# Kernel optimization log

Hardware: AMD Instinct MI355X
Metric: run time of the kernel (lower is better)

Reference implementation:

```python
import jax, jax.numpy as jnp
import numpy as np


def sign_ste(x):
    # forward-only module: plain sign (STE only matters for backward)
    return jnp.sign(x)


def fake_quant8(w):
    # per-tensor abs-max int8 fake quantization (scale is a buffer, not differentiated)
    scale = jax.lax.stop_gradient(jnp.max(jnp.abs(w)) / 127.0 + 1e-8)
    q = jnp.clip(jnp.round(w / scale), -128.0, 127.0)
    return q * scale


def conv2d(x, w):
    # VALID 3x3 conv, NCHW / OIHW, no bias
    return jax.lax.conv_general_dilated(
        x, w, window_strides=(1, 1), padding='VALID',
        dimension_numbers=('NCHW', 'OIHW', 'NCHW'))


def avg_pool2(x):
    # AvgPool2d(kernel=2, stride=2); spatial dims are even (22 -> 11)
    B, C, H, W = x.shape
    return x.reshape(B, C, H // 2, 2, W // 2, 2).mean(axis=(3, 5))


def setup_inputs() -> dict:
    key = jax.random.key(0)
    k = jax.random.split(key, 6)
    B = 8192
    x = jax.random.normal(k[0], (B, 1, 28, 28), dtype=jnp.float32)
    w1 = jax.random.normal(k[1], (16, 1, 3, 3), dtype=jnp.float32) * 0.1
    w2 = jax.random.normal(k[2], (16, 16, 3, 3), dtype=jnp.float32) * 0.1
    w3 = jax.random.normal(k[3], (32, 16, 3, 3), dtype=jnp.float32) * 0.1
    w_fc = jax.random.normal(k[4], (10, 32 * 11 * 11), dtype=jnp.float32) * 0.02
    b_fc = jax.random.normal(k[5], (10,), dtype=jnp.float32) * 0.02
    return {'x': x, 'w1': w1, 'w2': w2, 'w3': w3, 'w_fc': w_fc, 'b_fc': b_fc}


def reference(x, w1, w2, w3, w_fc, b_fc):
    h = fake_quant8(conv2d(x, w1))          # [B,16,26,26] int8 fake-quant
    h = sign_ste(h)                          # binarized activations
    h = sign_ste(conv2d(h, sign_ste(w2)))    # [B,16,24,24] binarized conv
    h = sign_ste(conv2d(h, sign_ste(w3)))    # [B,32,22,22] binarized conv
    h = avg_pool2(h)                         # [B,32,11,11]
    h = h.reshape(h.shape[0], -1)            # [B,3872]
    return h @ sign_ste(w_fc).T + b_fc       # [B,10]
```

## Files before the change

kernel.cpp:

```cpp
#include <hip/hip_runtime.h>
#include <stdint.h>


typedef int int4v __attribute__((ext_vector_type(4)));
typedef float f2 __attribute__((ext_vector_type(2)));

__device__ __forceinline__ int4v mfma_i8(int4v a, int4v b, int4v c) {
  return __builtin_amdgcn_mfma_i32_16x16x64_i8(a, b, c, 0, 0, 0);
}

__device__ __forceinline__ int dot4(int a, int b, int c) {
#if __has_builtin(__builtin_amdgcn_sdot4)
  return __builtin_amdgcn_sdot4(a, b, c, false);
#else
  int r = c;
  r += (int)(int8_t)(a)       * (int)(int8_t)(b);
  r += (int)(int8_t)(a >> 8)  * (int)(int8_t)(b >> 8);
  r += (int)(int8_t)(a >> 16) * (int)(int8_t)(b >> 16);
  r += (int)(int8_t)(a >> 24) * (int)(int8_t)(b >> 24);
  return r;
#endif
}

__device__ __forceinline__ int pack4(int r0, int r1, int r2, int r3) {
  const int t0 = __builtin_amdgcn_perm(r1, r0, 0x00000400);
  const int t1 = __builtin_amdgcn_perm(r3, r2, 0x00000400);
  return __builtin_amdgcn_perm(t1, t0, 0x05040100);
}

__device__ __forceinline__ int cl02(int v) {
  v = (v > 0) ? v : 0;
  v = (v < 2) ? v : 2;
  return v;
}

__device__ __forceinline__ int sgn_pack_byte(float v) {
  return (v > 0.f) - (v < 0.f);
}

__global__ __launch_bounds__(256) void k_prep_max(
    const float* __restrict__ x, const float* __restrict__ w1,
    const float* __restrict__ w2, const float* __restrict__ w3,
    const float* __restrict__ wfc, const float* __restrict__ bfc,
    int* __restrict__ ws, int B, int NMAX) {
  __shared__ __align__(16) float xs[1568];
  __shared__ __align__(8) float w1t[144];
  __shared__ float wred[4];
  __shared__ int part[4];

  const int tid = threadIdx.x;
  if ((int)blockIdx.x < NMAX) {
    const int img0 = blockIdx.x * 2;
    const bool has1 = (img0 + 1) < B;
    {
      const float4* x4a = (const float4*)(x + (size_t)img0 * 784);
      const float4* x4b = (const float4*)(x + (size_t)(img0 + (int)has1) * 784);
      for (int u = tid; u < 392; u += 256) {
        const int im = (u >= 196), i = im ? u - 196 : u;
        const float4 v = im ? x4b[i] : x4a[i];
        *(float4*)&xs[im * 784 + i * 4] = v;
      }
    }
    if (tid < 144) w1t[(tid % 9) * 16 + tid / 9] = w1[tid];
    __syncthreads();
    const f2* w1t2 = (const f2*)w1t;
    const float* xs0 = xs;
    const float* xs1 = xs + 784;
    float m = 0.f;
    for (int px = tid; px < 676; px += 256) {
      const int oy = px / 26, ox = px - oy * 26;
      float xw0[9], xw1[9];
#pragma unroll
      for (int r = 0; r < 3; ++r)
#pragma unroll
        for (int cc = 0; cc < 3; ++cc) {
          const int ix = (oy + r) * 28 + ox + cc;
          xw0[r * 3 + cc] = xs0[ix];
          xw1[r * 3 + cc] = xs1[ix];
        }
#pragma unroll
      for (int cw = 0; cw < 8; ++cw) {
        f2 h0 = {0.f, 0.f}, h1 = {0.f, 0.f};
#pragma unroll
        for (int i = 0; i < 9; ++i) {
          const f2 w = w1t2[i * 8 + cw];
          const f2 s0 = {xw0[i], xw0[i]};
          const f2 s1 = {xw1[i], xw1[i]};
          h0 += w * s0;
          h1 += w * s1;
        }
        m = fmaxf(m, fmaxf(fmaxf(fabsf(h0.x), fabsf(h0.y)),
                           fmaxf(fabsf(h1.x), fabsf(h1.y))));
      }
    }
#pragma unroll
    for (int off = 32; off; off >>= 1) m = fmaxf(m, __shfl_down(m, off, 64));
    if ((tid & 63) == 0) wred[tid >> 6] = m;
    __syncthreads();
    if (tid == 0) {
      const float mm = fmaxf(fmaxf(wred[0], wred[1]), fmaxf(wred[2], wred[3]));
      atomicMax(ws + ((int)blockIdx.x & 31), (int)__float_as_uint(mm));
    }
    return;
  }

  const int pb = blockIdx.x - NMAX;
  if (pb < 10) {
    const int j = pb;
    int s = 0;
    for (int i = tid; i < 3872; i += 256) {
      const float v = wfc[j * 3872 + i];
      s += (v > 0.f) - (v < 0.f);
    }
#pragma unroll
    for (int off = 32; off; off >>= 1) s += __shfl_down(s, off, 64);
    if ((tid & 63) == 0) part[tid >> 6] = s;
    __syncthreads();
    if (tid == 0) {
      const int rs = part[0] + part[1] + part[2] + part[3];
      ((float*)ws)[64 + j] = bfc[j] - (float)rs;
    }
    if (pb == 1 && tid < 16) {
      int s2 = 0;
      for (int i = 0; i < 144; ++i) s2 += sgn_pack_byte(w2[tid * 144 + i]);
      ws[80 + tid] = s2;
    }
    if (pb == 2 && tid < 32) {
      int s3 = 0;
      for (int i = 0; i < 144; ++i) s3 += sgn_pack_byte(w3[tid * 144 + i]);
      ws[96 + tid] = s3;
    }
    return;
  }
  int* dst = ws + 128;
  const int widx = (pb - 10) * 256 + tid;
  if (widx < 576) {
    const int oc = widx / 36, r = widx % 36, wp = r >> 2, icg = r & 3;
    unsigned wrd = 0;
#pragma unroll
    for (int b = 0; b < 4; ++b) {
      const float v = w2[(oc * 16 + icg * 4 + b) * 9 + wp];
      wrd |= ((unsigned)(uint8_t)(int8_t)sgn_pack_byte(v)) << (8 * b);
    }
    dst[widx] = (int)wrd;
  } else if (widx < 1728) {
    const int t = widx - 576;
    const int oc = t / 36, r = t % 36, wp = r >> 2, icg = r & 3;
    unsigned wrd = 0;
#pragma unroll
    for (int b = 0; b < 4; ++b) {
      const float v = w3[(oc * 16 + icg * 4 + b) * 9 + wp];
      wrd |= ((unsigned)(uint8_t)(int8_t)sgn_pack_byte(v)) << (8 * b);
    }
    dst[widx] = (int)wrd;
  } else if (widx < 11408) {
    const int t = widx - 1728;
    const int j = t / 968, r = t % 968, pos = r >> 3, cg = r & 7;
    unsigned wrd = 0;
#pragma unroll
    for (int b = 0; b < 4; ++b) {
      const float v = wfc[j * 3872 + (cg * 4 + b) * 121 + pos];
      wrd |= ((unsigned)(uint8_t)(int8_t)sgn_pack_byte(v)) << (8 * b);
    }
    dst[widx] = (int)wrd;
  }
}

__global__ __launch_bounds__(256) void k_forward(
    const float* __restrict__ x, const float* __restrict__ w1,
    const int* __restrict__ wsd,
    float* __restrict__ out, int B) {
  __shared__ __align__(16) char smem[40144];
  constexpr int RIMG = 20032;
  int* out_acc = (int*)(smem + 40064);

  const int* wpack = wsd + 128;
  const int* sw = wsd + 1856;
  const float* badj = (const float*)(wsd + 64);

  const int tid = threadIdx.x;
  const int img0 = blockIdx.x * 2;
  const bool has1 = (img0 + 1) < B;

  {
    const float4* x4a = (const float4*)(x + (size_t)img0 * 784);
    const float4* x4b = (const float4*)(x + (size_t)(img0 + (int)has1) * 784);
    for (int u = tid; u < 392; u += 256) {
      const int img = (u >= 196), i = img ? u - 196 : u;
      const float4 v = img ? x4b[i] : x4a[i];
      *(float4*)(smem + img * RIMG + 10816 + i * 16) = v;
    }
  }
  if (tid < 144) *(float*)(smem + 13952 + ((tid % 9) * 16 + tid / 9) * 4) = w1[tid];
  if (tid < 20) out_acc[tid] = 0;
  __syncthreads();

  float mraw = __uint_as_float((unsigned)wsd[0]);
#pragma unroll
  for (int k = 1; k < 32; ++k) mraw = fmaxf(mraw, __uint_as_float((unsigned)wsd[k]));
  const float scale = mraw / 127.0f + 1e-8f;
  const float thr = 0.5f * scale;
  const f2* w1t2 = (const f2*)(smem + 13952);
  const float* xs0 = (const float*)(smem + 10816);
  const float* xs1 = (const float*)(smem + RIMG + 10816);
  for (int px = tid; px < 676; px += 256) {
    const int oy = px / 26, ox = px - oy * 26;
    float xw0[9], xw1[9];
#pragma unroll
    for (int r = 0; r < 3; ++r)
#pragma unroll
      for (int cc = 0; cc < 3; ++cc) {
        const int ix = (oy + r) * 28 + ox + cc;
        xw0[r * 3 + cc] = xs0[ix];
        xw1[r * 3 + cc] = xs1[ix];
      }
    unsigned wq0[4] = {0u, 0u, 0u, 0u}, wq1[4] = {0u, 0u, 0u, 0u};
#pragma unroll
    for (int cw = 0; cw < 8; ++cw) {
      f2 h0 = {0.f, 0.f}, h1 = {0.f, 0.f};
#pragma unroll
      for (int i = 0; i < 9; ++i) {
        const f2 w = w1t2[i * 8 + cw];
        const f2 s0 = {xw0[i], xw0[i]};
        const f2 s1 = {xw1[i], xw1[i]};
        h0 += w * s0;
        h1 += w * s1;
      }
      wq0[cw >> 1] |= ((unsigned)((h0.x >= -thr) + (h0.x > thr))) << (8 * ((2 * cw) & 3));
      wq0[cw >> 1] |= ((unsigned)((h0.y >= -thr) + (h0.y > thr))) << (8 * ((2 * cw + 1) & 3));
      wq1[cw >> 1] |= ((unsigned)((h1.x >= -thr) + (h1.x > thr))) << (8 * ((2 * cw) & 3));
      wq1[cw >> 1] |= ((unsigned)((h1.y >= -thr) + (h1.y > thr))) << (8 * ((2 * cw + 1) & 3));
    }
    *(int4*)(smem + px * 16) =
        make_int4((int)wq0[0], (int)wq0[1], (int)wq0[2], (int)wq0[3]);
    *(int4*)(smem + RIMG + px * 16) =
        make_int4((int)wq1[0], (int)wq1[1], (int)wq1[2], (int)wq1[3]);
  }
  __syncthreads();

  const int lane = tid & 63, wv = tid >> 6;
  const int col = lane & 15, quad = lane >> 4;
  int dAct2[3], dAct3[3];
#pragma unroll
  for (int t = 0; t < 3; ++t) {
    const int wp = t * 4 + quad;
    dAct2[t] = ((wp / 3) * 26 + wp % 3) * 16;
    dAct3[t] = ((wp / 3) * 24 + wp % 3) * 16;
  }
  const bool kq0 = (quad == 0);

  {
    const int* wb = wpack + col * 36;
    int4v WA[3];
    WA[0] = *(const int4v*)(wb + quad * 4);
    WA[1] = *(const int4v*)(wb + 16 + quad * 4);
    WA[2] = kq0 ? *(const int4v*)(wb + 32) : (int4v){0, 0, 0, 0};
    const int4v acc0 = (int4v){1, 1, 1, 1} - *(const int4v*)(wsd + 80 + quad * 4);
#pragma unroll
    for (int img = 0; img < 2; ++img) {
      const int8_t* a1b = (const int8_t*)(smem + img * RIMG);
      int p0 = wv * 16 + col;
      int oy = p0 / 24, ox = p0 - oy * 24;
      const int8_t* abase = a1b + (oy * 26 + ox) * 16;
      int* h2p = (int*)(smem + img * RIMG + 10816 + p0 * 16 + quad * 4);
      for (int it = 0; it < 9; ++it) {
        int4v acc = acc0;
        acc = mfma_i8(WA[0], *(const int4v*)(abase + dAct2[0]), acc);
        acc = mfma_i8(WA[1], *(const int4v*)(abase + dAct2[1]), acc);
        acc = mfma_i8(WA[2], *(const int4v*)(abase + dAct2[2]), acc);
        *h2p = pack4(cl02(acc[0]), cl02(acc[1]), cl02(acc[2]), cl02(acc[3]));
        h2p += 256;
        abase += 1088;
        ox += 16;
        if (ox >= 24) { ox -= 24; abase += 32; }
      }
    }
  }
  __syncthreads();

  {
    int4v WA[2][3];
    int4v ac0[2];
#pragma unroll
    for (int ot = 0; ot < 2; ++ot) {
      const int* wb = wpack + 576 + (ot * 16 + col) * 36;
      WA[ot][0] = *(const int4v*)(wb + quad * 4);
      WA[ot][1] = *(const int4v*)(wb + 16 + quad * 4);
      WA[ot][2] = kq0 ? *(const int4v*)(wb + 32) : (int4v){0, 0, 0, 0};
      ac0[ot] = (int4v){1, 1, 1, 1} - *(const int4v*)(wsd + 96 + ot * 16 + quad * 4);
    }
    const int sub = col & 3;
    const int sy = sub >> 1, sx = sub & 1;
    const int cell0 = wv * 4 + (col >> 2);
    const int cy0 = cell0 / 11, cx0 = cell0 - cy0 * 11;
    const int aoff0 = ((cy0 * 2 + sy) * 24 + cx0 * 2 + sx) * 16;
    const int pb0 = cell0 * 8 + quad;
    const int aoffcap = ((20 + sy) * 24 + 20 + sx) * 16;
    const int pbcap = 120 * 8 + quad;
    const bool wlane = (sub == 0);
#pragma unroll
    for (int img = 0; img < 2; ++img) {
      const int8_t* h2b = (const int8_t*)(smem + img * RIMG + 10816);
      int* p4 = (int*)(smem + img * RIMG);
      int aoff = aoff0, pb = pb0, cx = cx0;
      for (int pt = wv; pt < 31; pt += 4) {
        const int8_t* abase = h2b + ((aoff < aoffcap) ? aoff : aoffcap);
        const int pbu = (pb < pbcap) ? pb : pbcap;
        const int4v B0 = *(const int4v*)(abase + dAct3[0]);
        const int4v B1 = *(const int4v*)(abase + dAct3[1]);
        const int4v B2 = *(const int4v*)(abase + dAct3[2]);
#pragma unroll
        for (int ot = 0; ot < 2; ++ot) {
          int4v acc = ac0[ot];
          acc = mfma_i8(WA[ot][0], B0, acc);
          acc = mfma_i8(WA[ot][1], B1, acc);
          acc = mfma_i8(WA[ot][2], B2, acc);
          int s = pack4(cl02(acc[0]), cl02(acc[1]), cl02(acc[2]), cl02(acc[3]));
          s += __builtin_amdgcn_update_dpp(0, s, 0xB1, 0xF, 0xF, false);
          s += __builtin_amdgcn_update_dpp(0, s, 0x4E, 0xF, 0xF, false);
          if (wlane) p4[pbu + ot * 4] = s;
        }
        aoff += 928;
        pb += 128;
        cx += 5;
        if (cx >= 11) { cx -= 11; aoff += 416; }
      }
    }
  }
  __syncthreads();

  for (int u = tid; u < 500; u += 256) {
    const int img = u / 250, r = u - img * 250;
    const int j = r / 25, k = r - j * 25;
    const int4* p44 = (const int4*)(smem + img * RIMG);
    int acc = 0;
    for (int pos = k; pos < 121; pos += 25) {
      const int4 pa = p44[pos * 2];
      const int4 pb = p44[pos * 2 + 1];
      const int* swr = sw + j * 968 + pos * 8;
      const int4 wa = *(const int4*)(swr);
      const int4 wbv = *(const int4*)(swr + 4);
      acc = dot4(pa.x, wa.x, acc);
      acc = dot4(pa.y, wa.y, acc);
      acc = dot4(pa.z, wa.z, acc);
      acc = dot4(pa.w, wa.w, acc);
      acc = dot4(pb.x, wbv.x, acc);
      acc = dot4(pb.y, wbv.y, acc);
      acc = dot4(pb.z, wbv.z, acc);
      acc = dot4(pb.w, wbv.w, acc);
    }
    atomicAdd(&out_acc[img * 10 + j], acc);
  }
  __syncthreads();
  if (tid < 20) {
    const int img = tid / 10, j = tid - img * 10;
    if (img == 0 || has1)
      out[(size_t)(img0 + img) * 10 + j] = 0.25f * (float)out_acc[tid] + badj[j];
  }
}

extern "C" void kernel_launch(void* const* d_in, const int* in_sizes, int n_in,
                              void* d_out, int out_size, void* d_ws, size_t ws_size,
                              hipStream_t stream) {
  const float* x   = (const float*)d_in[0];
  const float* w1  = (const float*)d_in[1];
  const float* w2  = (const float*)d_in[2];
  const float* w3  = (const float*)d_in[3];
  const float* wfc = (const float*)d_in[4];
  const float* bfc = (const float*)d_in[5];
  float* out = (float*)d_out;
  int* wsd = (int*)d_ws;
  const int B = in_sizes[0] / 784;
  const int NMAX = (B + 1) / 2;

  hipLaunchKernelGGL(k_prep_max, dim3(NMAX + 56), dim3(256), 0, stream,
                     x, w1, w2, w3, wfc, bfc, wsd, B, NMAX);
  hipLaunchKernelGGL(k_forward, dim3((B + 1) / 2), dim3(256), 0, stream, x, w1,
                     (const int*)wsd, out, B);
}
```

Measured before the change: 202.9 us.

## Process one image per block with halved LDS and padded conv2 output layout

Each block now processes one image instead of two, which halves shared memory (about 20KB) and doubles the grid so more blocks can be resident per CU. The conv1 loop is reordered to hold weights for one channel pair in registers across three pixel passes. The conv2 output row stride is padded from 24 to 25 positions, likely to reduce LDS bank conflicts in the conv3 reads. In exchange, per-block fixed costs (the weight loads and the scale max reduction) are paid twice as often.

Measured after the change: 194.4 us. 4.2% less time.

```diff
diff --git a/kernel.cpp b/kernel.cpp
--- a/kernel.cpp
+++ b/kernel.cpp
@@ -170,29 +170,22 @@
     const float* __restrict__ x, const float* __restrict__ w1,
     const int* __restrict__ wsd,
     float* __restrict__ out, int B) {
-  __shared__ __align__(16) char smem[40144];
-  constexpr int RIMG = 20032;
-  int* out_acc = (int*)(smem + 40064);
+  __shared__ __align__(16) char smem[20456];
+  int* out_acc = (int*)(smem + 20416);
 
   const int* wpack = wsd + 128;
   const int* sw = wsd + 1856;
   const float* badj = (const float*)(wsd + 64);
 
   const int tid = threadIdx.x;
-  const int img0 = blockIdx.x * 2;
-  const bool has1 = (img0 + 1) < B;
+  const int img = blockIdx.x;
 
   {
-    const float4* x4a = (const float4*)(x + (size_t)img0 * 784);
-    const float4* x4b = (const float4*)(x + (size_t)(img0 + (int)has1) * 784);
-    for (int u = tid; u < 392; u += 256) {
-      const int img = (u >= 196), i = img ? u - 196 : u;
-      const float4 v = img ? x4b[i] : x4a[i];
-      *(float4*)(smem + img * RIMG + 10816 + i * 16) = v;
-    }
+    const float4* x4 = (const float4*)(x + (size_t)img * 784);
+    if (tid < 196) *(float4*)(smem + 10816 + tid * 16) = x4[tid];
   }
   if (tid < 144) *(float*)(smem + 13952 + ((tid % 9) * 16 + tid / 9) * 4) = w1[tid];
-  if (tid < 20) out_acc[tid] = 0;
+  if (tid < 10) out_acc[tid] = 0;
   __syncthreads();
 
   float mraw = __uint_as_float((unsigned)wsd[0]);
@@ -200,41 +193,50 @@
   for (int k = 1; k < 32; ++k) mraw = fmaxf(mraw, __uint_as_float((unsigned)wsd[k]));
   const float scale = mraw / 127.0f + 1e-8f;
   const float thr = 0.5f * scale;
-  const f2* w1t2 = (const f2*)(smem + 13952);
-  const float* xs0 = (const float*)(smem + 10816);
-  const float* xs1 = (const float*)(smem + RIMG + 10816);
-  for (int px = tid; px < 676; px += 256) {
-    const int oy = px / 26, ox = px - oy * 26;
-    float xw0[9], xw1[9];
-#pragma unroll
-    for (int r = 0; r < 3; ++r)
-#pragma unroll
-      for (int cc = 0; cc < 3; ++cc) {
-        const int ix = (oy + r) * 28 + ox + cc;
-        xw0[r * 3 + cc] = xs0[ix];
-        xw1[r * 3 + cc] = xs1[ix];
-      }
-    unsigned wq0[4] = {0u, 0u, 0u, 0u}, wq1[4] = {0u, 0u, 0u, 0u};
-#pragma unroll
-    for (int cw = 0; cw < 8; ++cw) {
-      f2 h0 = {0.f, 0.f}, h1 = {0.f, 0.f};
+  {
+    const f2* w1t2 = (const f2*)(smem + 13952);
+    const float* xs0 = (const float*)(smem + 10816);
+    unsigned wq[3][4] = {};
+#pragma unroll
+    for (int ch = 0; ch < 4; ++ch) {
+      f2 wa[9], wb[9];
 #pragma unroll
       for (int i = 0; i < 9; ++i) {
-        const f2 w = w1t2[i * 8 + cw];
-        const f2 s0 = {xw0[i], xw0[i]};
-        const f2 s1 = {xw1[i], xw1[i]};
-        h0 += w * s0;
-        h1 += w * s1;
-      }
-      wq0[cw >> 1] |= ((unsigned)((h0.x >= -thr) + (h0.x > thr))) << (8 * ((2 * cw) & 3));
-      wq0[cw >> 1] |= ((unsigned)((h0.y >= -thr) + (h0.y > thr))) << (8 * ((2 * cw + 1) & 3));
-      wq1[cw >> 1] |= ((unsigned)((h1.x >= -thr) + (h1.x > thr))) << (8 * ((2 * cw) & 3));
-      wq1[cw >> 1] |= ((unsigned)((h1.y >= -thr) + (h1.y > thr))) << (8 * ((2 * cw + 1) & 3));
-    }
-    *(int4*)(smem + px * 16) =
-        make_int4((int)wq0[0], (int)wq0[1], (int)wq0[2], (int)wq0[3]);
-    *(int4*)(smem + RIMG + px * 16) =
-        make_int4((int)wq1[0], (int)wq1[1], (int)wq1[2], (int)wq1[3]);
+        wa[i] = w1t2[i * 8 + 2 * ch];
+        wb[i] = w1t2[i * 8 + 2 * ch + 1];
+      }
+#pragma unroll
+      for (int pi = 0; pi < 3; ++pi) {
+        const int px = tid + pi * 256;
+        if (px < 676) {
+          const int oy = px / 26, ox = px - oy * 26;
+          float xw[9];
+#pragma unroll
+          for (int r = 0; r < 3; ++r)
+#pragma unroll
+            for (int cc = 0; cc < 3; ++cc)
+              xw[r * 3 + cc] = xs0[(oy + r) * 28 + ox + cc];
+          f2 h0 = {0.f, 0.f}, h1 = {0.f, 0.f};
+#pragma unroll
+          for (int i = 0; i < 9; ++i) {
+            const f2 s = {xw[i], xw[i]};
+            h0 += wa[i] * s;
+            h1 += wb[i] * s;
+          }
+          wq[pi][ch] |= ((unsigned)((h0.x >= -thr) + (h0.x > thr))) << 0;
+          wq[pi][ch] |= ((unsigned)((h0.y >= -thr) + (h0.y > thr))) << 8;
+          wq[pi][ch] |= ((unsigned)((h1.x >= -thr) + (h1.x > thr))) << 16;
+          wq[pi][ch] |= ((unsigned)((h1.y >= -thr) + (h1.y > thr))) << 24;
+        }
+      }
+    }
+#pragma unroll
+    for (int pi = 0; pi < 3; ++pi) {
+      const int px = tid + pi * 256;
+      if (px < 676)
+        *(int4*)(smem + px * 16) =
+            make_int4((int)wq[pi][0], (int)wq[pi][1], (int)wq[pi][2], (int)wq[pi][3]);
+    }
   }
   __syncthreads();
 
@@ -245,7 +247,7 @@
   for (int t = 0; t < 3; ++t) {
     const int wp = t * 4 + quad;
     dAct2[t] = ((wp / 3) * 26 + wp % 3) * 16;
-    dAct3[t] = ((wp / 3) * 24 + wp % 3) * 16;
+    dAct3[t] = ((wp / 3) * 25 + wp % 3) * 16;
   }
   const bool kq0 = (quad == 0);
 
@@ -256,24 +258,21 @@
     WA[1] = *(const int4v*)(wb + 16 + quad * 4);
     WA[2] = kq0 ? *(const int4v*)(wb + 32) : (int4v){0, 0, 0, 0};
     const int4v acc0 = (int4v){1, 1, 1, 1} - *(const int4v*)(wsd + 80 + quad * 4);
-#pragma unroll
-    for (int img = 0; img < 2; ++img) {
-      const int8_t* a1b = (const int8_t*)(smem + img * RIMG);
-      int p0 = wv * 16 + col;
-      int oy = p0 / 24, ox = p0 - oy * 24;
-      const int8_t* abase = a1b + (oy * 26 + ox) * 16;
-      int* h2p = (int*)(smem + img * RIMG + 10816 + p0 * 16 + quad * 4);
-      for (int it = 0; it < 9; ++it) {
-        int4v acc = acc0;
-        acc = mfma_i8(WA[0], *(const int4v*)(abase + dAct2[0]), acc);
-        acc = mfma_i8(WA[1], *(const int4v*)(abase + dAct2[1]), acc);
-        acc = mfma_i8(WA[2], *(const int4v*)(abase + dAct2[2]), acc);
-        *h2p = pack4(cl02(acc[0]), cl02(acc[1]), cl02(acc[2]), cl02(acc[3]));
-        h2p += 256;
-        abase += 1088;
-        ox += 16;
-        if (ox >= 24) { ox -= 24; abase += 32; }
-      }
+    const int8_t* a1b = (const int8_t*)smem;
+    const int p0 = wv * 16 + col;
+    int oy = p0 / 24, ox = p0 - oy * 24;
+    const int8_t* abase = a1b + (oy * 26 + ox) * 16;
+    int* h2p = (int*)smem + 2704 + (oy * 25 + ox) * 4 + quad;
+    for (int it = 0; it < 9; ++it) {
+      int4v acc = acc0;
+      acc = mfma_i8(WA[0], *(const int4v*)(abase + dAct2[0]), acc);
+      acc = mfma_i8(WA[1], *(const int4v*)(abase + dAct2[1]), acc);
+      acc = mfma_i8(WA[2], *(const int4v*)(abase + dAct2[2]), acc);
+      *h2p = pack4(cl02(acc[0]), cl02(acc[1]), cl02(acc[2]), cl02(acc[3]));
+      abase += 1088;
+      h2p += 264;
+      ox += 16;
+      if (ox >= 24) { ox -= 24; abase += 32; h2p += 4; }
     }
   }
   __syncthreads();
@@ -293,46 +292,42 @@
     const int sy = sub >> 1, sx = sub & 1;
     const int cell0 = wv * 4 + (col >> 2);
     const int cy0 = cell0 / 11, cx0 = cell0 - cy0 * 11;
-    const int aoff0 = ((cy0 * 2 + sy) * 24 + cx0 * 2 + sx) * 16;
+    const int aoff0 = ((cy0 * 2 + sy) * 25 + cx0 * 2 + sx) * 16;
     const int pb0 = cell0 * 8 + quad;
-    const int aoffcap = ((20 + sy) * 24 + 20 + sx) * 16;
+    const int aoffcap = ((20 + sy) * 25 + 20 + sx) * 16;
     const int pbcap = 120 * 8 + quad;
     const bool wlane = (sub == 0);
-#pragma unroll
-    for (int img = 0; img < 2; ++img) {
-      const int8_t* h2b = (const int8_t*)(smem + img * RIMG + 10816);
-      int* p4 = (int*)(smem + img * RIMG);
-      int aoff = aoff0, pb = pb0, cx = cx0;
-      for (int pt = wv; pt < 31; pt += 4) {
-        const int8_t* abase = h2b + ((aoff < aoffcap) ? aoff : aoffcap);
-        const int pbu = (pb < pbcap) ? pb : pbcap;
-        const int4v B0 = *(const int4v*)(abase + dAct3[0]);
-        const int4v B1 = *(const int4v*)(abase + dAct3[1]);
-        const int4v B2 = *(const int4v*)(abase + dAct3[2]);
-#pragma unroll
-        for (int ot = 0; ot < 2; ++ot) {
-          int4v acc = ac0[ot];
-          acc = mfma_i8(WA[ot][0], B0, acc);
-          acc = mfma_i8(WA[ot][1], B1, acc);
-          acc = mfma_i8(WA[ot][2], B2, acc);
-          int s = pack4(cl02(acc[0]), cl02(acc[1]), cl02(acc[2]), cl02(acc[3]));
-          s += __builtin_amdgcn_update_dpp(0, s, 0xB1, 0xF, 0xF, false);
-          s += __builtin_amdgcn_update_dpp(0, s, 0x4E, 0xF, 0xF, false);
-          if (wlane) p4[pbu + ot * 4] = s;
-        }
-        aoff += 928;
-        pb += 128;
-        cx += 5;
-        if (cx >= 11) { cx -= 11; aoff += 416; }
-      }
-    }
-  }
-  __syncthreads();
-
-  for (int u = tid; u < 500; u += 256) {
-    const int img = u / 250, r = u - img * 250;
-    const int j = r / 25, k = r - j * 25;
-    const int4* p44 = (const int4*)(smem + img * RIMG);
+    const int8_t* h2b = (const int8_t*)(smem + 10816);
+    int* p4 = (int*)smem;
+    int aoff = aoff0, pb = pb0, cx = cx0;
+    for (int pt = wv; pt < 31; pt += 4) {
+      const int8_t* abase = h2b + ((aoff < aoffcap) ? aoff : aoffcap);
+      const int pbu = (pb < pbcap) ? pb : pbcap;
+      const int4v B0 = *(const int4v*)(abase + dAct3[0]);
+      const int4v B1 = *(const int4v*)(abase + dAct3[1]);
+      const int4v B2 = *(const int4v*)(abase + dAct3[2]);
+#pragma unroll
+      for (int ot = 0; ot < 2; ++ot) {
+        int4v acc = ac0[ot];
+        acc = mfma_i8(WA[ot][0], B0, acc);
+        acc = mfma_i8(WA[ot][1], B1, acc);
+        acc = mfma_i8(WA[ot][2], B2, acc);
+        int s = pack4(cl02(acc[0]), cl02(acc[1]), cl02(acc[2]), cl02(acc[3]));
+        s += __builtin_amdgcn_update_dpp(0, s, 0xB1, 0xF, 0xF, false);
+        s += __builtin_amdgcn_update_dpp(0, s, 0x4E, 0xF, 0xF, false);
+        if (wlane) p4[pbu + ot * 4] = s;
+      }
+      aoff += 960;
+      pb += 128;
+      cx += 5;
+      if (cx >= 11) { cx -= 11; aoff += 448; }
+    }
+  }
+  __syncthreads();
+
+  if (tid < 250) {
+    const int j = tid / 25, k = tid - j * 25;
+    const int4* p44 = (const int4*)smem;
     int acc = 0;
     for (int pos = k; pos < 121; pos += 25) {
       const int4 pa = p44[pos * 2];
@@ -349,14 +344,11 @@
       acc = dot4(pb.z, wbv.z, acc);
       acc = dot4(pb.w, wbv.w, acc);
     }
-    atomicAdd(&out_acc[img * 10 + j], acc);
-  }
-  __syncthreads();
-  if (tid < 20) {
-    const int img = tid / 10, j = tid - img * 10;
-    if (img == 0 || has1)
-      out[(size_t)(img0 + img) * 10 + j] = 0.25f * (float)out_acc[tid] + badj[j];
-  }
+    atomicAdd(&out_acc[j], acc);
+  }
+  __syncthreads();
+  if (tid < 10)
+    out[(size_t)img * 10 + tid] = 0.25f * (float)out_acc[tid] + badj[tid];
 }
 
 extern "C" void kernel_launch(void* const* d_in, const int* in_sizes, int n_in,
@@ -375,6 +367,6 @@
 
   hipLaunchKernelGGL(k_prep_max, dim3(NMAX + 56), dim3(256), 0, stream,
                      x, w1, w2, w3, wfc, bfc, wsd, B, NMAX);
-  hipLaunchKernelGGL(k_forward, dim3((B + 1) / 2), dim3(256), 0, stream, x, w1,
+  hipLaunchKernelGGL(k_forward, dim3(B), dim3(256), 0, stream, x, w1,
                      (const int*)wsd, out, B);
 }
```
